# Optimization experiments

Hardware: AMD Instinct MI355X
Metric: run time of the kernel (lower is better)

## Reference

```python
import jax, jax.numpy as jnp
import numpy as np

DIM = 6
HID = 8
N_UT = DIM * (DIM - 1) // 2  # 15


def setup_inputs() -> dict:
    key = jax.random.key(0)
    ks = jax.random.split(key, 13)
    B, T = 256, 4096
    x = jax.random.normal(ks[0], (B, T, DIM), dtype=jnp.float32)

    def kaiming(k, fan_out, fan_in):
        std = np.sqrt(2.0 / fan_in)
        return jax.random.normal(k, (fan_out, fan_in), dtype=jnp.float32) * std

    inp = {
        "x": x,
        "W_in": kaiming(ks[1], HID, DIM),
        "b_in": jnp.zeros((HID,), jnp.float32),
        "W1": kaiming(ks[2], HID, HID), "b1": jnp.zeros((HID,), jnp.float32),
        "W2": kaiming(ks[3], HID, HID), "b2": jnp.zeros((HID,), jnp.float32),
        "W3": kaiming(ks[4], HID, HID), "b3": jnp.zeros((HID,), jnp.float32),
        "W4": kaiming(ks[5], HID, HID), "b4": jnp.zeros((HID,), jnp.float32),
        "W_out": kaiming(ks[6], N_UT, HID),
        "b_out": jnp.zeros((N_UT,), jnp.float32),
    }
    return inp


def reference(x, W_in, b_in, W1, b1, W2, b2, W3, b3, W4, b4, W_out, b_out):
    B, T, dim = x.shape
    xf = x.reshape(B * T, dim)
    sp = jax.nn.softplus
    y = sp(xf @ W_in.T + b_in)
    y = sp(y @ W1.T + b1)
    y = sp(y @ W2.T + b2)
    y = sp(y @ W3.T + b3)
    y = sp(y @ W4.T + b4)
    ut = y @ W_out.T + b_out  # [N, dim*(dim-1)/2]
    iu, ju = jnp.triu_indices(dim, k=1)  # row-major order matches torch loop
    L = jnp.zeros((B * T, dim, dim), dtype=x.dtype)
    L = L.at[:, iu, ju].set(ut)
    L = L.at[:, ju, iu].set(-ut)
    return L.reshape(B, T, dim, dim)
```

## Files before the change

kernel.cpp:

```cpp
#include <hip/hip_runtime.h>

#define DEV_INLINE __device__ __forceinline__

typedef float vfloat4 __attribute__((ext_vector_type(4)));

DEV_INLINE float softplus_f(float v) {
#if __has_builtin(__builtin_amdgcn_logf) && __has_builtin(__builtin_amdgcn_exp2f)
    float e = __builtin_amdgcn_exp2f(fabsf(v) * -1.44269504f);
    float l = __builtin_amdgcn_logf(1.0f + e);
    return fmaf(0.69314718f, l, fmaxf(v, 0.0f));
#else
    return fmaxf(v, 0.0f) + __logf(1.0f + __expf(-fabsf(v)));
#endif
}

__global__ __launch_bounds__(256) void pb_kernel(
    const float* __restrict__ x,
    const float* __restrict__ W_in, const float* __restrict__ b_in,
    const float* __restrict__ W1,   const float* __restrict__ b1,
    const float* __restrict__ W2,   const float* __restrict__ b2,
    const float* __restrict__ W3,   const float* __restrict__ b3,
    const float* __restrict__ W4,   const float* __restrict__ b4,
    const float* __restrict__ W_out,const float* __restrict__ b_out,
    float* __restrict__ out, int n_rows)
{
    __shared__ vfloat4 sbuf[4][64 * 9];

    const int tid  = threadIdx.x;
    const int wave = tid >> 6;
    const int lane = tid & 63;
    const int row_raw = blockIdx.x * 256 + tid;
    const int row = row_raw < n_rows ? row_raw : n_rows - 1;

    const float2* xv = (const float2*)(x + (size_t)row * 6);
    float2 p0 = xv[0], p1 = xv[1], p2 = xv[2];
    const float xin[6] = { p0.x, p0.y, p1.x, p1.y, p2.x, p2.y };

    float y[8];
    #pragma unroll
    for (int o = 0; o < 8; ++o) {
        float acc = b_in[o];
        #pragma unroll
        for (int i = 0; i < 6; ++i)
            acc = fmaf(W_in[o * 6 + i], xin[i], acc);
        y[o] = softplus_f(acc);
    }

    const float* Ws[4] = { W1, W2, W3, W4 };
    const float* bs[4] = { b1, b2, b3, b4 };
    #pragma unroll
    for (int l = 0; l < 4; ++l) {
        const float* __restrict__ W = Ws[l];
        const float* __restrict__ b = bs[l];
        float t[8];
        #pragma unroll
        for (int o = 0; o < 8; ++o) {
            float acc = b[o];
            #pragma unroll
            for (int i = 0; i < 8; ++i)
                acc = fmaf(W[o * 8 + i], y[i], acc);
            t[o] = softplus_f(acc);
        }
        #pragma unroll
        for (int o = 0; o < 8; ++o) y[o] = t[o];
    }

    float u[15];
    #pragma unroll
    for (int o = 0; o < 15; ++o) {
        float acc = b_out[o];
        #pragma unroll
        for (int i = 0; i < 8; ++i)
            acc = fmaf(W_out[o * 8 + i], y[i], acc);
        u[o] = acc;
    }

    float L[36];
    #pragma unroll
    for (int i = 0; i < 36; ++i) L[i] = 0.0f;
    {
        int k = 0;
        #pragma unroll
        for (int i = 0; i < 6; ++i) {
            #pragma unroll
            for (int j = i + 1; j < 6; ++j) {
                L[i * 6 + j] = u[k];
                L[j * 6 + i] = -u[k];
                ++k;
            }
        }
    }

    vfloat4* ws = sbuf[wave];
    #pragma unroll
    for (int m = 0; m < 9; ++m) {
        vfloat4 v = { L[4 * m + 0], L[4 * m + 1], L[4 * m + 2], L[4 * m + 3] };
        ws[lane * 9 + m] = v;
    }

    asm volatile("s_waitcnt lgkmcnt(0)" ::: "memory");

    vfloat4* dst = (vfloat4*)out + (size_t)blockIdx.x * (256 * 9) + wave * (64 * 9);
    #pragma unroll
    for (int q = 0; q < 9; ++q) {
        vfloat4 v = ws[q * 64 + lane];
        __builtin_nontemporal_store(v, &dst[q * 64 + lane]);
    }
}

extern "C" void kernel_launch(void* const* d_in, const int* in_sizes, int n_in,
                              void* d_out, int out_size, void* d_ws, size_t ws_size,
                              hipStream_t stream) {
    const float* x     = (const float*)d_in[0];
    const float* W_in  = (const float*)d_in[1];
    const float* b_in  = (const float*)d_in[2];
    const float* W1    = (const float*)d_in[3];
    const float* b1    = (const float*)d_in[4];
    const float* W2    = (const float*)d_in[5];
    const float* b2    = (const float*)d_in[6];
    const float* W3    = (const float*)d_in[7];
    const float* b3    = (const float*)d_in[8];
    const float* W4    = (const float*)d_in[9];
    const float* b4    = (const float*)d_in[10];
    const float* W_out = (const float*)d_in[11];
    const float* b_out = (const float*)d_in[12];
    float* out = (float*)d_out;

    const int n_rows = in_sizes[0] / 6;
    const int block = 256;
    const int grid = (n_rows + block - 1) / block;

    hipLaunchKernelGGL(pb_kernel, dim3(grid), dim3(block), 0, stream,
                       x, W_in, b_in, W1, b1, W2, b2, W3, b3, W4, b4,
                       W_out, b_out, out, n_rows);
}
```

Measured before the change: 198.9 us.

## Process four rows per thread to amortize weight loads across rows

```diff
diff --git a/kernel.cpp b/kernel.cpp
--- a/kernel.cpp
+++ b/kernel.cpp
@@ -14,7 +14,7 @@
 #endif
 }
 
-__global__ __launch_bounds__(256) void pb_kernel(
+__global__ __launch_bounds__(256, 4) void pb_kernel(
     const float* __restrict__ x,
     const float* __restrict__ W_in, const float* __restrict__ b_in,
     const float* __restrict__ W1,   const float* __restrict__ b1,
@@ -29,21 +29,30 @@
     const int tid  = threadIdx.x;
     const int wave = tid >> 6;
     const int lane = tid & 63;
-    const int row_raw = blockIdx.x * 256 + tid;
-    const int row = row_raw < n_rows ? row_raw : n_rows - 1;
+    const long long blockbase = (long long)blockIdx.x * 1024;
 
-    const float2* xv = (const float2*)(x + (size_t)row * 6);
-    float2 p0 = xv[0], p1 = xv[1], p2 = xv[2];
-    const float xin[6] = { p0.x, p0.y, p1.x, p1.y, p2.x, p2.y };
+    float xin[4][6];
+    #pragma unroll
+    for (int s = 0; s < 4; ++s) {
+        const long long row = blockbase + s * 256 + tid;
+        const float2* xv = (const float2*)(x + row * 6);
+        float2 p0 = xv[0], p1 = xv[1], p2 = xv[2];
+        xin[s][0] = p0.x; xin[s][1] = p0.y;
+        xin[s][2] = p1.x; xin[s][3] = p1.y;
+        xin[s][4] = p2.x; xin[s][5] = p2.y;
+    }
 
-    float y[8];
+    float y[4][8];
     #pragma unroll
     for (int o = 0; o < 8; ++o) {
-        float acc = b_in[o];
         #pragma unroll
-        for (int i = 0; i < 6; ++i)
-            acc = fmaf(W_in[o * 6 + i], xin[i], acc);
-        y[o] = softplus_f(acc);
+        for (int s = 0; s < 4; ++s) {
+            float acc = b_in[o];
+            #pragma unroll
+            for (int i = 0; i < 6; ++i)
+                acc = fmaf(W_in[o * 6 + i], xin[s][i], acc);
+            y[s][o] = softplus_f(acc);
+        }
     }
 
     const float* Ws[4] = { W1, W2, W3, W4 };
@@ -52,59 +61,69 @@
     for (int l = 0; l < 4; ++l) {
         const float* __restrict__ W = Ws[l];
         const float* __restrict__ b = bs[l];
-        float t[8];
+        float t[4][8];
         #pragma unroll
         for (int o = 0; o < 8; ++o) {
-            float acc = b[o];
             #pragma unroll
-            for (int i = 0; i < 8; ++i)
-                acc = fmaf(W[o * 8 + i], y[i], acc);
-            t[o] = softplus_f(acc);
+            for (int s = 0; s < 4; ++s) {
+                float acc = b[o];
+                #pragma unroll
+                for (int i = 0; i < 8; ++i)
+                    acc = fmaf(W[o * 8 + i], y[s][i], acc);
+                t[s][o] = softplus_f(acc);
+            }
         }
         #pragma unroll
-        for (int o = 0; o < 8; ++o) y[o] = t[o];
-    }
-
-    float u[15];
-    #pragma unroll
-    for (int o = 0; o < 15; ++o) {
-        float acc = b_out[o];
-        #pragma unroll
-        for (int i = 0; i < 8; ++i)
-            acc = fmaf(W_out[o * 8 + i], y[i], acc);
-        u[o] = acc;
-    }
-
-    float L[36];
-    #pragma unroll
-    for (int i = 0; i < 36; ++i) L[i] = 0.0f;
-    {
-        int k = 0;
-        #pragma unroll
-        for (int i = 0; i < 6; ++i) {
+        for (int s = 0; s < 4; ++s)
             #pragma unroll
-            for (int j = i + 1; j < 6; ++j) {
-                L[i * 6 + j] = u[k];
-                L[j * 6 + i] = -u[k];
-                ++k;
-            }
-        }
+            for (int o = 0; o < 8; ++o)
+                y[s][o] = t[s][o];
     }
 
     vfloat4* ws = sbuf[wave];
     #pragma unroll
-    for (int m = 0; m < 9; ++m) {
-        vfloat4 v = { L[4 * m + 0], L[4 * m + 1], L[4 * m + 2], L[4 * m + 3] };
-        ws[lane * 9 + m] = v;
-    }
+    for (int s = 0; s < 4; ++s) {
+        float u[15];
+        #pragma unroll
+        for (int o = 0; o < 15; ++o) {
+            float acc = b_out[o];
+            #pragma unroll
+            for (int i = 0; i < 8; ++i)
+                acc = fmaf(W_out[o * 8 + i], y[s][i], acc);
+            u[o] = acc;
+        }
 
-    asm volatile("s_waitcnt lgkmcnt(0)" ::: "memory");
+        float L[36];
+        #pragma unroll
+        for (int i = 0; i < 36; ++i) L[i] = 0.0f;
+        {
+            int k = 0;
+            #pragma unroll
+            for (int i = 0; i < 6; ++i) {
+                #pragma unroll
+                for (int j = i + 1; j < 6; ++j) {
+                    L[i * 6 + j] = u[k];
+                    L[j * 6 + i] = -u[k];
+                    ++k;
+                }
+            }
+        }
 
-    vfloat4* dst = (vfloat4*)out + (size_t)blockIdx.x * (256 * 9) + wave * (64 * 9);
-    #pragma unroll
-    for (int q = 0; q < 9; ++q) {
-        vfloat4 v = ws[q * 64 + lane];
-        __builtin_nontemporal_store(v, &dst[q * 64 + lane]);
+        #pragma unroll
+        for (int m = 0; m < 9; ++m) {
+            vfloat4 v = { L[4 * m + 0], L[4 * m + 1], L[4 * m + 2], L[4 * m + 3] };
+            ws[lane * 9 + m] = v;
+        }
+
+        asm volatile("s_waitcnt lgkmcnt(0)" ::: "memory");
+
+        vfloat4* dst = (vfloat4*)out
+                     + (blockbase + s * 256 + wave * 64) * 9;
+        #pragma unroll
+        for (int q = 0; q < 9; ++q) {
+            vfloat4 v = ws[q * 64 + lane];
+            __builtin_nontemporal_store(v, &dst[q * 64 + lane]);
+        }
     }
 }
 
@@ -127,10 +146,10 @@
     float* out = (float*)d_out;
 
     const int n_rows = in_sizes[0] / 6;
-    const int block = 256;
-    const int grid = (n_rows + block - 1) / block;
+    const int rows_per_block = 1024;
+    const int grid = (n_rows + rows_per_block - 1) / rows_per_block;
 
-    hipLaunchKernelGGL(pb_kernel, dim3(grid), dim3(block), 0, stream,
+    hipLaunchKernelGGL(pb_kernel, dim3(grid), dim3(256), 0, stream,
                        x, W_in, b_in, W1, b1, W2, b2, W3, b3, W4, b4,
                        W_out, b_out, out, n_rows);
 }
```

Measured after the change: 204.4 us. 2.8% more time.
